# Optimization experiments

Hardware: AMD Instinct MI355X
Metric: run time of the kernel (lower is better)

The kernel has to match this reference:

```python
import jax, jax.numpy as jnp
import numpy as np

D_MODEL = 1024
N_HEADS = 16
HEAD_DIM = D_MODEL // N_HEADS  # 64
LATENT = 256
B, S = 2, 2048


def setup_inputs() -> dict:
    key = jax.random.key(0)
    ks = jax.random.split(key, 13)
    sc = 0.02
    inp = {
        'x': jax.random.normal(ks[0], (B, S, D_MODEL), jnp.float32),
        'Wq': jax.random.normal(ks[1], (D_MODEL, D_MODEL), jnp.float32) * sc,
        'bq': jnp.zeros((D_MODEL,), jnp.float32),
        'Wkd': jax.random.normal(ks[2], (D_MODEL, LATENT), jnp.float32) * sc,
        'bkd': jnp.zeros((LATENT,), jnp.float32),
        'Wvd': jax.random.normal(ks[3], (D_MODEL, LATENT), jnp.float32) * sc,
        'bvd': jnp.zeros((LATENT,), jnp.float32),
        'Wku': jax.random.normal(ks[4], (LATENT, D_MODEL), jnp.float32) * sc,
        'bku': jnp.zeros((D_MODEL,), jnp.float32),
        'Wvu': jax.random.normal(ks[5], (LATENT, D_MODEL), jnp.float32) * sc,
        'bvu': jnp.zeros((D_MODEL,), jnp.float32),
        'Wo': jax.random.normal(ks[6], (D_MODEL, D_MODEL), jnp.float32) * sc,
        'bo': jnp.zeros((D_MODEL,), jnp.float32),
    }
    return inp


def reference(x, Wq, bq, Wkd, bkd, Wvd, bvd, Wku, bku, Wvu, bvu, Wo, bo):
    b, s, _ = x.shape
    # projections
    Q = x @ Wq + bq                      # [b, s, d_model]
    K_latent = x @ Wkd + bkd             # [b, s, latent]
    V_latent = x @ Wvd + bvd             # [b, s, latent]
    K = K_latent @ Wku + bku             # [b, s, d_model]
    V = V_latent @ Wvu + bvu             # [b, s, d_model]
    # split heads
    Qh = Q.reshape(b, s, N_HEADS, HEAD_DIM)
    Kh = K.reshape(b, s, N_HEADS, HEAD_DIM)
    Vh = V.reshape(b, s, N_HEADS, HEAD_DIM)
    scale = 1.0 / jnp.sqrt(jnp.asarray(HEAD_DIM, x.dtype))
    scores = jnp.einsum('bqhd,bkhd->bhqk', Qh, Kh) * scale  # [b,h,s,s]
    attn = jax.nn.softmax(scores, axis=-1)
    ctx = jnp.einsum('bhqk,bkhd->bqhd', attn, Vh).reshape(b, s, D_MODEL)
    out = ctx @ Wo + bo
    return out
```

## Files before the change

kernel.cpp:

```cpp
#include <hip/hip_runtime.h>
#include <hip/hip_bf16.h>
#include <cstddef>

#define B_SZ 2
#define SEQ  2048
#define DM   1024
#define NH   16
#define HD   64
#define LAT  256
#define MTOT (B_SZ*SEQ)
#define NQKV 1536
#define QSCALE 0.18033688011112042f

typedef short bf16x8 __attribute__((ext_vector_type(8)));
typedef float floatx4 __attribute__((ext_vector_type(4)));
typedef float floatx16 __attribute__((ext_vector_type(16)));
typedef unsigned short u16;

#if __has_builtin(__builtin_amdgcn_exp2f)
#define EXP2(x) __builtin_amdgcn_exp2f(x)
#else
#define EXP2(x) exp2f(x)
#endif

__device__ __forceinline__ u16 f2bf(float f) {
  union { float f; unsigned u; } a; a.f = f;
  unsigned r = a.u + 0x7FFFu + ((a.u >> 16) & 1u);
  return (u16)(r >> 16);
}

__device__ __forceinline__ floatx4 mfma16(bf16x8 a, bf16x8 b, floatx4 c) {
  return __builtin_amdgcn_mfma_f32_16x16x32_bf16(a, b, c, 0, 0, 0);
}

__device__ __forceinline__ floatx16 mfma32(bf16x8 a, bf16x8 b, floatx16 c) {
  return __builtin_amdgcn_mfma_f32_32x32x16_bf16(a, b, c, 0, 0, 0);
}

__device__ __forceinline__ void load16(const u16* g, u16* l) {
  __builtin_amdgcn_global_load_lds((const __attribute__((address_space(1))) unsigned*)g,
                                   (__attribute__((address_space(3))) unsigned*)l, 16, 0, 0);
}

__device__ void transpose_tile(const float* __restrict__ W, u16* __restrict__ WT,
                               int K, int N, int k0, int n0, u16 (*t)[65]) {
  const int r = threadIdx.x >> 4;
  const int c4 = (threadIdx.x & 15) * 4;
#pragma unroll
  for (int s = 0; s < 4; s++) {
    int row = s * 16 + r;
    float4 v = *(const float4*)&W[(size_t)(k0 + row) * N + n0 + c4];
    t[row][c4 + 0] = f2bf(v.x); t[row][c4 + 1] = f2bf(v.y);
    t[row][c4 + 2] = f2bf(v.z); t[row][c4 + 3] = f2bf(v.w);
  }
  __syncthreads();
  const int r2 = threadIdx.x >> 2;
  const int c8 = (threadIdx.x & 3) * 16;
  __align__(16) u16 tmp[16];
#pragma unroll
  for (int i = 0; i < 16; i++) tmp[i] = t[c8 + i][r2];
  u16* dst = WT + (size_t)(n0 + r2) * K + k0 + c8;
  *(bf16x8*)dst       = *(const bf16x8*)&tmp[0];
  *(bf16x8*)(dst + 8) = *(const bf16x8*)&tmp[8];
}

__global__ __launch_bounds__(256)
void prep_k(const float* __restrict__ x, u16* __restrict__ xb,
            const float* __restrict__ Wq, const float* __restrict__ Wkd,
            const float* __restrict__ Wvd, const float* __restrict__ Wku,
            const float* __restrict__ Wvu, const float* __restrict__ Wo,
            u16* __restrict__ WstkT, u16* __restrict__ WkuT,
            u16* __restrict__ WvuT, u16* __restrict__ WoT,
            const float* __restrict__ bq, const float* __restrict__ bkd,
            const float* __restrict__ bvd, float* __restrict__ bqkv) {
  __shared__ u16 t[64][65];
  const int blk = blockIdx.x;
  if (blk < 4096) {
    int i = blk * 256 + threadIdx.x;
    float4 v = ((const float4*)x)[i];
    ushort4 o; o.x = f2bf(v.x); o.y = f2bf(v.y); o.z = f2bf(v.z); o.w = f2bf(v.w);
    ((ushort4*)xb)[i] = o;
  } else if (blk < 4352) {
    int tt = blk - 4096;
    transpose_tile(Wq, WstkT, DM, DM, (tt >> 4) * 64, (tt & 15) * 64, t);
  } else if (blk < 4416) {
    int tt = blk - 4352;
    transpose_tile(Wkd, WstkT + (size_t)DM * DM, DM, LAT, (tt >> 2) * 64, (tt & 3) * 64, t);
  } else if (blk < 4480) {
    int tt = blk - 4416;
    transpose_tile(Wvd, WstkT + (size_t)1280 * DM, DM, LAT, (tt >> 2) * 64, (tt & 3) * 64, t);
  } else if (blk < 4544) {
    int tt = blk - 4480;
    transpose_tile(Wku, WkuT, LAT, DM, (tt >> 4) * 64, (tt & 15) * 64, t);
  } else if (blk < 4608) {
    int tt = blk - 4544;
    transpose_tile(Wvu, WvuT, LAT, DM, (tt >> 4) * 64, (tt & 15) * 64, t);
  } else if (blk < 4864) {
    int tt = blk - 4608;
    transpose_tile(Wo, WoT, DM, DM, (tt >> 4) * 64, (tt & 15) * 64, t);
  } else {
    int i = (blk - 4864) * 256 + threadIdx.x;
    float v = (i < 1024) ? bq[i] : (i < 1280) ? bkd[i - 1024] : bvd[i - 1280];
    bqkv[i] = v;
  }
}

template<int TM, int OUT_BF16, int VT1>
__global__ __launch_bounds__(256)
void gemm_bt(const u16* __restrict__ A0, const u16* __restrict__ A1,
             const u16* __restrict__ BT0, const u16* __restrict__ BT1,
             const float* __restrict__ bias0, const float* __restrict__ bias1,
             void* __restrict__ C0, void* __restrict__ C1,
             int M, int N, int Kd, int lda, float qscale, int qcols) {
  constexpr int FM = TM / 32;
  __shared__ u16 As[TM * 64];
  __shared__ u16 Bs[64 * 64];
  const u16* A  = blockIdx.z ? A1 : A0;
  const u16* BT = blockIdx.z ? BT1 : BT0;
  const float* bias = blockIdx.z ? bias1 : bias0;
  void* C = blockIdx.z ? C1 : C0;

  const int tid = threadIdx.x;
  const int m0 = blockIdx.y * TM, n0 = blockIdx.x * 64;
  const int wave = tid >> 6, lane = tid & 63;
  const int l15 = lane & 15, quad = lane >> 4;
  const int wm = (wave >> 1) * (TM / 2), wn = (wave & 1) * 32;

  floatx4 acc[FM][2];
#pragma unroll
  for (int i = 0; i < FM; i++)
#pragma unroll
    for (int j = 0; j < 2; j++) acc[i][j] = (floatx4){0.f, 0.f, 0.f, 0.f};

  const int tr = tid >> 3;
  const int tc8 = (tid & 7) * 8;
  const u16* Ag = A  + (size_t)(m0 + tr) * lda + tc8;
  const u16* Bg = BT + (size_t)(n0 + tr) * Kd + tc8;
  u16* AsW = &As[(size_t)tid * 8];
  u16* BsW = &Bs[(size_t)tid * 8];

  for (int k0 = 0; k0 < Kd; k0 += 64) {
    __syncthreads();
#pragma unroll
    for (int s = 0; s < FM; s++)
      load16(Ag + (size_t)(s * 32) * lda + k0, AsW + s * 2048);
#pragma unroll
    for (int s = 0; s < 2; s++)
      load16(Bg + (size_t)(s * 32) * Kd  + k0, BsW + s * 2048);
    __syncthreads();
#pragma unroll
    for (int kk = 0; kk < 2; kk++) {
      bf16x8 af[FM], bfr[2];
#pragma unroll
      for (int i = 0; i < FM; i++)
        af[i]  = *(const bf16x8*)&As[(wm + i * 16 + l15) * 64 + kk * 32 + quad * 8];
#pragma unroll
      for (int j = 0; j < 2; j++)
        bfr[j] = *(const bf16x8*)&Bs[(wn + j * 16 + l15) * 64 + kk * 32 + quad * 8];
#pragma unroll
      for (int i = 0; i < FM; i++)
#pragma unroll
        for (int j = 0; j < 2; j++)
          acc[i][j] = mfma16(af[i], bfr[j], acc[i][j]);
    }
  }

  if (VT1 && blockIdx.z == 1) {
#pragma unroll
    for (int i = 0; i < FM; i++) {
      int row = m0 + wm + i * 16 + quad * 4;
      int bb = row >> 11, sb = row & 2047;
#pragma unroll
      for (int j = 0; j < 2; j++) {
        int col = n0 + wn + j * 16 + l15;
        float bv = bias[col];
        union { u16 u[4]; uint2 w2; } tv;
#pragma unroll
        for (int r = 0; r < 4; r++) tv.u[r] = f2bf(acc[i][j][r] + bv);
        *(uint2*)((u16*)C + ((size_t)(bb * 16 + (col >> 6)) * 64 + (col & 63)) * SEQ + sb) = tv.w2;
      }
    }
  } else {
#pragma unroll
    for (int i = 0; i < FM; i++) {
      int row = m0 + wm + i * 16 + quad * 4;
#pragma unroll
      for (int j = 0; j < 2; j++) {
        int col = n0 + wn + j * 16 + l15;
        float bv = bias[col];
        float sc = (col < qcols) ? qscale : 1.f;
#pragma unroll
        for (int r = 0; r < 4; r++) {
          float v = (acc[i][j][r] + bv) * sc;
          if (OUT_BF16) ((u16*)C)[(size_t)(row + r) * N + col] = f2bf(v);
          else          ((float*)C)[(size_t)(row + r) * N + col] = v;
        }
      }
    }
  }
}

__global__ __launch_bounds__(512, 3)
void attn_fused(const u16* __restrict__ Q, const u16* __restrict__ K,
                const u16* __restrict__ VT, u16* __restrict__ CTX) {
  __shared__ __align__(16) u16 KVt[2][2][2][64][64];
  const int lin = blockIdx.y * gridDim.x + blockIdx.x;
  const int idx = lin >> 3;
  const int bh = (lin & 7) * 4 + (idx >> 4);
  const int q0 = (idx & 15) * 128;
  const int b = bh >> 4, h = bh & 15;
  const int wave = threadIdx.x >> 6, lane = threadIdx.x & 63;
  const int qw = wave & 3;
  const int kw = wave >> 2;
  const int l31 = lane & 31;
  const int hi = lane >> 5;
  const int lr = lane >> 3;
  const int cx = (lane & 7) ^ lr;

  bf16x8 qf[4];
  {
    const u16* Qp = Q + (size_t)(b * SEQ + q0 + qw * 32 + l31) * NQKV + h * HD + hi * 8;
#pragma unroll
    for (int dc = 0; dc < 4; dc++)
      qf[dc] = *(const bf16x8*)(Qp + dc * 16);
  }

  const u16* Ks[2];
  const u16* Vs[2];
#pragma unroll
  for (int s = 0; s < 2; s++) {
    int r = qw * 8 + s * 32 + lr;
    Ks[s] = K + (size_t)(b * SEQ + kw * 1024 + r) * DM + h * HD + cx * 8;
    Vs[s] = VT + ((size_t)bh * HD + r) * SEQ + kw * 1024 + cx * 8;
  }

  floatx16 o[2];
  const floatx16 zf16 = {0.f,0.f,0.f,0.f,0.f,0.f,0.f,0.f,0.f,0.f,0.f,0.f,0.f,0.f,0.f,0.f};
  o[0] = zf16; o[1] = zf16;
  float ls = 0.f;

#pragma unroll
  for (int s = 0; s < 2; s++) {
    load16(Ks[s], &KVt[kw][0][0][qw * 8 + s * 32][0]);
    load16(Vs[s], &KVt[kw][0][1][qw * 8 + s * 32][0]);
  }
  __syncthreads();

#pragma unroll 2
  for (int t = 0; t < 16; ++t) {
    const int cur = t & 1, nxt = cur ^ 1;
    if (t < 15) {
      const int kt = (t + 1) * 64;
#pragma unroll
      for (int s = 0; s < 2; s++) {
        load16(Ks[s] + (size_t)kt * DM, &KVt[kw][nxt][0][qw * 8 + s * 32][0]);
        load16(Vs[s] + kt,              &KVt[kw][nxt][1][qw * 8 + s * 32][0]);
      }
    }
#pragma unroll
    for (int kh = 0; kh < 2; kh++) {
      const int rk = kh * 32 + l31;
      bf16x8 kf[4];
#pragma unroll
      for (int dc = 0; dc < 4; dc++)
        kf[dc] = *(const bf16x8*)&KVt[kw][cur][0][rk][((dc * 2 + hi) ^ (rk & 7)) * 8];
      floatx16 z = zf16;
      __builtin_amdgcn_s_setprio(1);
#pragma unroll
      for (int dc = 0; dc < 4; dc++) z = mfma32(kf[dc], qf[dc], z);
      __builtin_amdgcn_s_setprio(0);
      {
        float p0 = EXP2(z[0]), p1 = EXP2(z[1]), p2 = EXP2(z[2]), p3 = EXP2(z[3]);
        float p4 = EXP2(z[4]), p5 = EXP2(z[5]), p6 = EXP2(z[6]), p7 = EXP2(z[7]);
        ls += ((p0 + p1) + (p2 + p3)) + ((p4 + p5) + (p6 + p7));
        unsigned w0 = __builtin_amdgcn_perm(__float_as_uint(p1) + 0x8000u,
                                            __float_as_uint(p0) + 0x8000u, 0x07060302u);
        unsigned w1 = __builtin_amdgcn_perm(__float_as_uint(p3) + 0x8000u,
                                            __float_as_uint(p2) + 0x8000u, 0x07060302u);
        unsigned w2 = __builtin_amdgcn_perm(__float_as_uint(p5) + 0x8000u,
                                            __float_as_uint(p4) + 0x8000u, 0x07060302u);
        unsigned w3 = __builtin_amdgcn_perm(__float_as_uint(p7) + 0x8000u,
                                            __float_as_uint(p6) + 0x8000u, 0x07060302u);
        unsigned s0 = (unsigned)__shfl_xor((int)w0, 32);
        unsigned s1 = (unsigned)__shfl_xor((int)w1, 32);
        unsigned s2 = (unsigned)__shfl_xor((int)w2, 32);
        unsigned s3 = (unsigned)__shfl_xor((int)w3, 32);
        union { unsigned u[4]; bf16x8 v; } b0;
        b0.u[0] = hi ? s2 : w0;
        b0.u[1] = hi ? s3 : w1;
        b0.u[2] = hi ? w2 : s0;
        b0.u[3] = hi ? w3 : s1;
        bf16x8 vf0 = *(const bf16x8*)&KVt[kw][cur][1][l31     ][((kh * 4 + hi) ^ (l31 & 7)) * 8];
        bf16x8 vf1 = *(const bf16x8*)&KVt[kw][cur][1][32 + l31][((kh * 4 + hi) ^ (l31 & 7)) * 8];
        __builtin_amdgcn_s_setprio(1);
        o[0] = mfma32(vf0, b0.v, o[0]);
        o[1] = mfma32(vf1, b0.v, o[1]);
        __builtin_amdgcn_s_setprio(0);
      }
      {
        float p0 = EXP2(z[8]),  p1 = EXP2(z[9]),  p2 = EXP2(z[10]), p3 = EXP2(z[11]);
        float p4 = EXP2(z[12]), p5 = EXP2(z[13]), p6 = EXP2(z[14]), p7 = EXP2(z[15]);
        ls += ((p0 + p1) + (p2 + p3)) + ((p4 + p5) + (p6 + p7));
        unsigned w0 = __builtin_amdgcn_perm(__float_as_uint(p1) + 0x8000u,
                                            __float_as_uint(p0) + 0x8000u, 0x07060302u);
        unsigned w1 = __builtin_amdgcn_perm(__float_as_uint(p3) + 0x8000u,
                                            __float_as_uint(p2) + 0x8000u, 0x07060302u);
        unsigned w2 = __builtin_amdgcn_perm(__float_as_uint(p5) + 0x8000u,
                                            __float_as_uint(p4) + 0x8000u, 0x07060302u);
        unsigned w3 = __builtin_amdgcn_perm(__float_as_uint(p7) + 0x8000u,
                                            __float_as_uint(p6) + 0x8000u, 0x07060302u);
        unsigned s0 = (unsigned)__shfl_xor((int)w0, 32);
        unsigned s1 = (unsigned)__shfl_xor((int)w1, 32);
        unsigned s2 = (unsigned)__shfl_xor((int)w2, 32);
        unsigned s3 = (unsigned)__shfl_xor((int)w3, 32);
        union { unsigned u[4]; bf16x8 v; } b1;
        b1.u[0] = hi ? s2 : w0;
        b1.u[1] = hi ? s3 : w1;
        b1.u[2] = hi ? w2 : s0;
        b1.u[3] = hi ? w3 : s1;
        bf16x8 vf0 = *(const bf16x8*)&KVt[kw][cur][1][l31     ][((kh * 4 + 2 + hi) ^ (l31 & 7)) * 8];
        bf16x8 vf1 = *(const bf16x8*)&KVt[kw][cur][1][32 + l31][((kh * 4 + 2 + hi) ^ (l31 & 7)) * 8];
        __builtin_amdgcn_s_setprio(1);
        o[0] = mfma32(vf0, b1.v, o[0]);
        o[1] = mfma32(vf1, b1.v, o[1]);
        __builtin_amdgcn_s_setprio(0);
      }
    }
    __syncthreads();
  }

  float* Osh = (float*)&KVt[0][0][0][0][0];
  float* Lsh = Osh + 128 * 68;
  const float lsum = ls + __shfl_xor(ls, 32);
  const int q = qw * 32 + l31;
  if (kw == 1) {
#pragma unroll
    for (int dh = 0; dh < 2; dh++)
#pragma unroll
      for (int g = 0; g < 4; g++) {
        floatx4 tv = {o[dh][4 * g], o[dh][4 * g + 1], o[dh][4 * g + 2], o[dh][4 * g + 3]};
        *(floatx4*)&Osh[q * 68 + dh * 32 + g * 8 + hi * 4] = tv;
      }
    if (hi == 0) Lsh[q] = lsum;
  }
  __syncthreads();
  if (kw == 0) {
    const float inv = 1.f / (lsum + Lsh[q]);
    u16* Crow = CTX + (size_t)(b * SEQ + q0 + q) * DM + h * HD + hi * 4;
#pragma unroll
    for (int dh = 0; dh < 2; dh++)
#pragma unroll
      for (int g = 0; g < 4; g++) {
        const float* oc = &Osh[q * 68 + dh * 32 + g * 8 + hi * 4];
        union { u16 u[4]; uint2 w2; } tv;
#pragma unroll
        for (int r = 0; r < 4; r++)
          tv.u[r] = f2bf((o[dh][4 * g + r] + oc[r]) * inv);
        *(uint2*)(Crow + dh * 32 + g * 8) = tv.w2;
      }
  }
}

extern "C" void kernel_launch(void* const* d_in, const int* in_sizes, int n_in,
                              void* d_out, int out_size, void* d_ws, size_t ws_size,
                              hipStream_t stream) {
  const float* x   = (const float*)d_in[0];
  const float* Wq  = (const float*)d_in[1];
  const float* bq  = (const float*)d_in[2];
  const float* Wkd = (const float*)d_in[3];
  const float* bkd = (const float*)d_in[4];
  const float* Wvd = (const float*)d_in[5];
  const float* bvd = (const float*)d_in[6];
  const float* Wku = (const float*)d_in[7];
  const float* bku = (const float*)d_in[8];
  const float* Wvu = (const float*)d_in[9];
  const float* bvu = (const float*)d_in[10];
  const float* Wo  = (const float*)d_in[11];
  const float* bo  = (const float*)d_in[12];
  float* out = (float*)d_out;

  float* bqkv = (float*)d_ws;
  u16* p = (u16*)((char*)d_ws + 1536 * sizeof(float));
  u16* xb    = p; p += (size_t)MTOT * DM;
  u16* WstkT = p; p += (size_t)NQKV * DM;
  u16* WkuT  = p; p += (size_t)DM * LAT;
  u16* WvuT  = p; p += (size_t)DM * LAT;
  u16* WoT   = p; p += (size_t)DM * DM;
  u16* QKVb  = p; p += (size_t)MTOT * NQKV;
  u16* Kb    = p; p += (size_t)MTOT * DM;
  u16* VTb   = p; p += (size_t)MTOT * DM;
  u16* CXb   = p; p += (size_t)MTOT * DM;

  prep_k<<<4870, 256, 0, stream>>>(x, xb, Wq, Wkd, Wvd, Wku, Wvu, Wo,
                                   WstkT, WkuT, WvuT, WoT, bq, bkd, bvd, bqkv);

  gemm_bt<128, 1, 0><<<dim3(NQKV / 64, MTOT / 128, 1), 256, 0, stream>>>(
      xb, xb, WstkT, WstkT, bqkv, bqkv, QKVb, QKVb, MTOT, NQKV, DM, DM, QSCALE, DM);
  gemm_bt<128, 1, 1><<<dim3(DM / 64, MTOT / 128, 2), 256, 0, stream>>>(
      QKVb + 1024, QKVb + 1280, WkuT, WvuT, bku, bvu, Kb, VTb, MTOT, DM, LAT, NQKV, 1.f, 0);

  attn_fused<<<dim3(SEQ / 128, B_SZ * NH), 512, 0, stream>>>(QKVb, Kb, VTb, CXb);

  gemm_bt<64, 0, 0><<<dim3(DM / 64, MTOT / 64, 1), 256, 0, stream>>>(
      CXb, CXb, WoT, WoT, bo, bo, out, out, MTOT, DM, DM, DM, 1.f, 0);
}
```

Measured before the change: 207.0 us.

## Give each attention wave two query sub-tiles to reuse K/V fragments

Halves the attention block from 512 to 256 threads, so each wave now handles 64 query rows (two 32-row sub-tiles) instead of 32. Each K and V fragment read from LDS feeds twice as many MFMAs, and each thread issues four async loads per tile instead of two. The aim is less LDS read traffic per FLOP and fewer waves contending per block. The cost is higher register pressure (four output accumulators, two score tiles), fewer waves to hide latency, and a changed launch bound of (256, 2).

New measurement: 204.7 us. Within noise of the previous version (-1.1%).

```diff
diff --git a/kernel.cpp b/kernel.cpp
--- a/kernel.cpp
+++ b/kernel.cpp
@@ -40,6 +40,28 @@
 __device__ __forceinline__ void load16(const u16* g, u16* l) {
   __builtin_amdgcn_global_load_lds((const __attribute__((address_space(1))) unsigned*)g,
                                    (__attribute__((address_space(3))) unsigned*)l, 16, 0, 0);
+}
+
+__device__ __forceinline__ bf16x8 packex(float p0, float p1, float p2, float p3,
+                                         float p4, float p5, float p6, float p7, int hi) {
+  unsigned w0 = __builtin_amdgcn_perm(__float_as_uint(p1) + 0x8000u,
+                                      __float_as_uint(p0) + 0x8000u, 0x07060302u);
+  unsigned w1 = __builtin_amdgcn_perm(__float_as_uint(p3) + 0x8000u,
+                                      __float_as_uint(p2) + 0x8000u, 0x07060302u);
+  unsigned w2 = __builtin_amdgcn_perm(__float_as_uint(p5) + 0x8000u,
+                                      __float_as_uint(p4) + 0x8000u, 0x07060302u);
+  unsigned w3 = __builtin_amdgcn_perm(__float_as_uint(p7) + 0x8000u,
+                                      __float_as_uint(p6) + 0x8000u, 0x07060302u);
+  unsigned s0 = (unsigned)__shfl_xor((int)w0, 32);
+  unsigned s1 = (unsigned)__shfl_xor((int)w1, 32);
+  unsigned s2 = (unsigned)__shfl_xor((int)w2, 32);
+  unsigned s3 = (unsigned)__shfl_xor((int)w3, 32);
+  union { unsigned u[4]; bf16x8 v; } bb;
+  bb.u[0] = hi ? s2 : w0;
+  bb.u[1] = hi ? s3 : w1;
+  bb.u[2] = hi ? w2 : s0;
+  bb.u[3] = hi ? w3 : s1;
+  return bb.v;
 }
 
 __device__ void transpose_tile(const float* __restrict__ W, u16* __restrict__ WT,
@@ -200,7 +222,7 @@
   }
 }
 
-__global__ __launch_bounds__(512, 3)
+__global__ __launch_bounds__(256, 2)
 void attn_fused(const u16* __restrict__ Q, const u16* __restrict__ K,
                 const u16* __restrict__ VT, u16* __restrict__ CTX) {
   __shared__ __align__(16) u16 KVt[2][2][2][64][64];
@@ -210,39 +232,35 @@
   const int q0 = (idx & 15) * 128;
   const int b = bh >> 4, h = bh & 15;
   const int wave = threadIdx.x >> 6, lane = threadIdx.x & 63;
-  const int qw = wave & 3;
-  const int kw = wave >> 2;
+  const int qw = wave & 1;
+  const int kw = wave >> 1;
   const int l31 = lane & 31;
   const int hi = lane >> 5;
   const int lr = lane >> 3;
   const int cx = (lane & 7) ^ lr;
 
-  bf16x8 qf[4];
+  bf16x8 qf0[4], qf1[4];
   {
-    const u16* Qp = Q + (size_t)(b * SEQ + q0 + qw * 32 + l31) * NQKV + h * HD + hi * 8;
-#pragma unroll
-    for (int dc = 0; dc < 4; dc++)
-      qf[dc] = *(const bf16x8*)(Qp + dc * 16);
-  }
-
-  const u16* Ks[2];
-  const u16* Vs[2];
-#pragma unroll
-  for (int s = 0; s < 2; s++) {
-    int r = qw * 8 + s * 32 + lr;
-    Ks[s] = K + (size_t)(b * SEQ + kw * 1024 + r) * DM + h * HD + cx * 8;
-    Vs[s] = VT + ((size_t)bh * HD + r) * SEQ + kw * 1024 + cx * 8;
-  }
-
-  floatx16 o[2];
+    const u16* Qp = Q + (size_t)(b * SEQ + q0 + qw * 64 + l31) * NQKV + h * HD + hi * 8;
+#pragma unroll
+    for (int dc = 0; dc < 4; dc++) {
+      qf0[dc] = *(const bf16x8*)(Qp + dc * 16);
+      qf1[dc] = *(const bf16x8*)(Qp + (size_t)32 * NQKV + dc * 16);
+    }
+  }
+
+  const u16* Kbase = K + (size_t)(b * SEQ + kw * 1024 + qw * 32 + lr) * DM + h * HD + cx * 8;
+  const u16* Vbase = VT + ((size_t)bh * HD + qw * 32 + lr) * SEQ + kw * 1024 + cx * 8;
+
+  floatx16 o00, o01, o10, o11;
   const floatx16 zf16 = {0.f,0.f,0.f,0.f,0.f,0.f,0.f,0.f,0.f,0.f,0.f,0.f,0.f,0.f,0.f,0.f};
-  o[0] = zf16; o[1] = zf16;
-  float ls = 0.f;
-
-#pragma unroll
-  for (int s = 0; s < 2; s++) {
-    load16(Ks[s], &KVt[kw][0][0][qw * 8 + s * 32][0]);
-    load16(Vs[s], &KVt[kw][0][1][qw * 8 + s * 32][0]);
+  o00 = zf16; o01 = zf16; o10 = zf16; o11 = zf16;
+  float ls0 = 0.f, ls1 = 0.f;
+
+#pragma unroll
+  for (int s = 0; s < 4; s++) {
+    load16(Kbase + (size_t)(s * 8) * DM, &KVt[kw][0][0][qw * 32 + s * 8][0]);
+    load16(Vbase + (size_t)(s * 8) * SEQ, &KVt[kw][0][1][qw * 32 + s * 8][0]);
   }
   __syncthreads();
 
@@ -252,9 +270,9 @@
     if (t < 15) {
       const int kt = (t + 1) * 64;
 #pragma unroll
-      for (int s = 0; s < 2; s++) {
-        load16(Ks[s] + (size_t)kt * DM, &KVt[kw][nxt][0][qw * 8 + s * 32][0]);
-        load16(Vs[s] + kt,              &KVt[kw][nxt][1][qw * 8 + s * 32][0]);
+      for (int s = 0; s < 4; s++) {
+        load16(Kbase + (size_t)(kt + s * 8) * DM, &KVt[kw][nxt][0][qw * 32 + s * 8][0]);
+        load16(Vbase + (size_t)(s * 8) * SEQ + kt, &KVt[kw][nxt][1][qw * 32 + s * 8][0]);
       }
     }
 #pragma unroll
@@ -264,65 +282,48 @@
 #pragma unroll
       for (int dc = 0; dc < 4; dc++)
         kf[dc] = *(const bf16x8*)&KVt[kw][cur][0][rk][((dc * 2 + hi) ^ (rk & 7)) * 8];
-      floatx16 z = zf16;
+      floatx16 z0 = zf16, z1 = zf16;
       __builtin_amdgcn_s_setprio(1);
 #pragma unroll
-      for (int dc = 0; dc < 4; dc++) z = mfma32(kf[dc], qf[dc], z);
+      for (int dc = 0; dc < 4; dc++) {
+        z0 = mfma32(kf[dc], qf0[dc], z0);
+        z1 = mfma32(kf[dc], qf1[dc], z1);
+      }
       __builtin_amdgcn_s_setprio(0);
+      bf16x8 vfA0 = *(const bf16x8*)&KVt[kw][cur][1][l31     ][((kh * 4 + hi) ^ (l31 & 7)) * 8];
+      bf16x8 vfA1 = *(const bf16x8*)&KVt[kw][cur][1][32 + l31][((kh * 4 + hi) ^ (l31 & 7)) * 8];
+      bf16x8 vfB0 = *(const bf16x8*)&KVt[kw][cur][1][l31     ][((kh * 4 + 2 + hi) ^ (l31 & 7)) * 8];
+      bf16x8 vfB1 = *(const bf16x8*)&KVt[kw][cur][1][32 + l31][((kh * 4 + 2 + hi) ^ (l31 & 7)) * 8];
       {
-        float p0 = EXP2(z[0]), p1 = EXP2(z[1]), p2 = EXP2(z[2]), p3 = EXP2(z[3]);
-        float p4 = EXP2(z[4]), p5 = EXP2(z[5]), p6 = EXP2(z[6]), p7 = EXP2(z[7]);
-        ls += ((p0 + p1) + (p2 + p3)) + ((p4 + p5) + (p6 + p7));
-        unsigned w0 = __builtin_amdgcn_perm(__float_as_uint(p1) + 0x8000u,
-                                            __float_as_uint(p0) + 0x8000u, 0x07060302u);
-        unsigned w1 = __builtin_amdgcn_perm(__float_as_uint(p3) + 0x8000u,
-                                            __float_as_uint(p2) + 0x8000u, 0x07060302u);
-        unsigned w2 = __builtin_amdgcn_perm(__float_as_uint(p5) + 0x8000u,
-                                            __float_as_uint(p4) + 0x8000u, 0x07060302u);
-        unsigned w3 = __builtin_amdgcn_perm(__float_as_uint(p7) + 0x8000u,
-                                            __float_as_uint(p6) + 0x8000u, 0x07060302u);
-        unsigned s0 = (unsigned)__shfl_xor((int)w0, 32);
-        unsigned s1 = (unsigned)__shfl_xor((int)w1, 32);
-        unsigned s2 = (unsigned)__shfl_xor((int)w2, 32);
-        unsigned s3 = (unsigned)__shfl_xor((int)w3, 32);
-        union { unsigned u[4]; bf16x8 v; } b0;
-        b0.u[0] = hi ? s2 : w0;
-        b0.u[1] = hi ? s3 : w1;
-        b0.u[2] = hi ? w2 : s0;
-        b0.u[3] = hi ? w3 : s1;
-        bf16x8 vf0 = *(const bf16x8*)&KVt[kw][cur][1][l31     ][((kh * 4 + hi) ^ (l31 & 7)) * 8];
-        bf16x8 vf1 = *(const bf16x8*)&KVt[kw][cur][1][32 + l31][((kh * 4 + hi) ^ (l31 & 7)) * 8];
+        float p0 = EXP2(z0[0]), p1 = EXP2(z0[1]), p2 = EXP2(z0[2]), p3 = EXP2(z0[3]);
+        float p4 = EXP2(z0[4]), p5 = EXP2(z0[5]), p6 = EXP2(z0[6]), p7 = EXP2(z0[7]);
+        float p8 = EXP2(z0[8]),  p9 = EXP2(z0[9]),  pa = EXP2(z0[10]), pb = EXP2(z0[11]);
+        float pc = EXP2(z0[12]), pd = EXP2(z0[13]), pe = EXP2(z0[14]), pf = EXP2(z0[15]);
+        ls0 += (((p0 + p1) + (p2 + p3)) + ((p4 + p5) + (p6 + p7)))
+             + (((p8 + p9) + (pa + pb)) + ((pc + pd) + (pe + pf)));
+        bf16x8 bA = packex(p0, p1, p2, p3, p4, p5, p6, p7, hi);
+        bf16x8 bB = packex(p8, p9, pa, pb, pc, pd, pe, pf, hi);
         __builtin_amdgcn_s_setprio(1);
-        o[0] = mfma32(vf0, b0.v, o[0]);
-        o[1] = mfma32(vf1, b0.v, o[1]);
+        o00 = mfma32(vfA0, bA, o00);
+        o01 = mfma32(vfA1, bA, o01);
+        o00 = mfma32(vfB0, bB, o00);
+        o01 = mfma32(vfB1, bB, o01);
         __builtin_amdgcn_s_setprio(0);
       }
       {
-        float p0 = EXP2(z[8]),  p1 = EXP2(z[9]),  p2 = EXP2(z[10]), p3 = EXP2(z[11]);
-        float p4 = EXP2(z[12]), p5 = EXP2(z[13]), p6 = EXP2(z[14]), p7 = EXP2(z[15]);
-        ls += ((p0 + p1) + (p2 + p3)) + ((p4 + p5) + (p6 + p7));
-        unsigned w0 = __builtin_amdgcn_perm(__float_as_uint(p1) + 0x8000u,
-                                            __float_as_uint(p0) + 0x8000u, 0x07060302u);
-        unsigned w1 = __builtin_amdgcn_perm(__float_as_uint(p3) + 0x8000u,
-                                            __float_as_uint(p2) + 0x8000u, 0x07060302u);
-        unsigned w2 = __builtin_amdgcn_perm(__float_as_uint(p5) + 0x8000u,
-                                            __float_as_uint(p4) + 0x8000u, 0x07060302u);
-        unsigned w3 = __builtin_amdgcn_perm(__float_as_uint(p7) + 0x8000u,
-                                            __float_as_uint(p6) + 0x8000u, 0x07060302u);
-        unsigned s0 = (unsigned)__shfl_xor((int)w0, 32);
-        unsigned s1 = (unsigned)__shfl_xor((int)w1, 32);
-        unsigned s2 = (unsigned)__shfl_xor((int)w2, 32);
-        unsigned s3 = (unsigned)__shfl_xor((int)w3, 32);
-        union { unsigned u[4]; bf16x8 v; } b1;
-        b1.u[0] = hi ? s2 : w0;
-        b1.u[1] = hi ? s3 : w1;
-        b1.u[2] = hi ? w2 : s0;
-        b1.u[3] = hi ? w3 : s1;
-        bf16x8 vf0 = *(const bf16x8*)&KVt[kw][cur][1][l31     ][((kh * 4 + 2 + hi) ^ (l31 & 7)) * 8];
-        bf16x8 vf1 = *(const bf16x8*)&KVt[kw][cur][1][32 + l31][((kh * 4 + 2 + hi) ^ (l31 & 7)) * 8];
+        float p0 = EXP2(z1[0]), p1 = EXP2(z1[1]), p2 = EXP2(z1[2]), p3 = EXP2(z1[3]);
+        float p4 = EXP2(z1[4]), p5 = EXP2(z1[5]), p6 = EXP2(z1[6]), p7 = EXP2(z1[7]);
+        float p8 = EXP2(z1[8]),  p9 = EXP2(z1[9]),  pa = EXP2(z1[10]), pb = EXP2(z1[11]);
+        float pc = EXP2(z1[12]), pd = EXP2(z1[13]), pe = EXP2(z1[14]), pf = EXP2(z1[15]);
+        ls1 += (((p0 + p1) + (p2 + p3)) + ((p4 + p5) + (p6 + p7)))
+             + (((p8 + p9) + (pa + pb)) + ((pc + pd) + (pe + pf)));
+        bf16x8 bA = packex(p0, p1, p2, p3, p4, p5, p6, p7, hi);
+        bf16x8 bB = packex(p8, p9, pa, pb, pc, pd, pe, pf, hi);
         __builtin_amdgcn_s_setprio(1);
-        o[0] = mfma32(vf0, b1.v, o[0]);
-        o[1] = mfma32(vf1, b1.v, o[1]);
+        o10 = mfma32(vfA0, bA, o10);
+        o11 = mfma32(vfA1, bA, o11);
+        o10 = mfma32(vfB0, bB, o10);
+        o11 = mfma32(vfB1, bB, o11);
         __builtin_amdgcn_s_setprio(0);
       }
     }
@@ -331,33 +332,49 @@
 
   float* Osh = (float*)&KVt[0][0][0][0][0];
   float* Lsh = Osh + 128 * 68;
-  const float lsum = ls + __shfl_xor(ls, 32);
-  const int q = qw * 32 + l31;
+  const float lsum0 = ls0 + __shfl_xor(ls0, 32);
+  const float lsum1 = ls1 + __shfl_xor(ls1, 32);
+  const int qA = qw * 64 + l31;
+  const int qB = qw * 64 + 32 + l31;
   if (kw == 1) {
 #pragma unroll
-    for (int dh = 0; dh < 2; dh++)
-#pragma unroll
-      for (int g = 0; g < 4; g++) {
-        floatx4 tv = {o[dh][4 * g], o[dh][4 * g + 1], o[dh][4 * g + 2], o[dh][4 * g + 3]};
-        *(floatx4*)&Osh[q * 68 + dh * 32 + g * 8 + hi * 4] = tv;
-      }
-    if (hi == 0) Lsh[q] = lsum;
+    for (int g = 0; g < 4; g++) {
+      *(floatx4*)&Osh[qA * 68 +      g * 8 + hi * 4] =
+          (floatx4){o00[4*g], o00[4*g+1], o00[4*g+2], o00[4*g+3]};
+      *(floatx4*)&Osh[qA * 68 + 32 + g * 8 + hi * 4] =
+          (floatx4){o01[4*g], o01[4*g+1], o01[4*g+2], o01[4*g+3]};
+      *(floatx4*)&Osh[qB * 68 +      g * 8 + hi * 4] =
+          (floatx4){o10[4*g], o10[4*g+1], o10[4*g+2], o10[4*g+3]};
+      *(floatx4*)&Osh[qB * 68 + 32 + g * 8 + hi * 4] =
+          (floatx4){o11[4*g], o11[4*g+1], o11[4*g+2], o11[4*g+3]};
+    }
+    if (hi == 0) { Lsh[qA] = lsum0; Lsh[qB] = lsum1; }
   }
   __syncthreads();
   if (kw == 0) {
-    const float inv = 1.f / (lsum + Lsh[q]);
-    u16* Crow = CTX + (size_t)(b * SEQ + q0 + q) * DM + h * HD + hi * 4;
-#pragma unroll
-    for (int dh = 0; dh < 2; dh++)
-#pragma unroll
-      for (int g = 0; g < 4; g++) {
-        const float* oc = &Osh[q * 68 + dh * 32 + g * 8 + hi * 4];
-        union { u16 u[4]; uint2 w2; } tv;
-#pragma unroll
-        for (int r = 0; r < 4; r++)
-          tv.u[r] = f2bf((o[dh][4 * g + r] + oc[r]) * inv);
-        *(uint2*)(Crow + dh * 32 + g * 8) = tv.w2;
-      }
+    const float inv0 = 1.f / (lsum0 + Lsh[qA]);
+    const float inv1 = 1.f / (lsum1 + Lsh[qB]);
+    u16* CrowA = CTX + (size_t)(b * SEQ + q0 + qA) * DM + h * HD + hi * 4;
+    u16* CrowB = CTX + (size_t)(b * SEQ + q0 + qB) * DM + h * HD + hi * 4;
+#pragma unroll
+    for (int g = 0; g < 4; g++) {
+      const float* ocA0 = &Osh[qA * 68 +      g * 8 + hi * 4];
+      const float* ocA1 = &Osh[qA * 68 + 32 + g * 8 + hi * 4];
+      const float* ocB0 = &Osh[qB * 68 +      g * 8 + hi * 4];
+      const float* ocB1 = &Osh[qB * 68 + 32 + g * 8 + hi * 4];
+      union { u16 u[4]; uint2 w2; } t0, t1, t2, t3;
+#pragma unroll
+      for (int r = 0; r < 4; r++) {
+        t0.u[r] = f2bf((o00[4*g+r] + ocA0[r]) * inv0);
+        t1.u[r] = f2bf((o01[4*g+r] + ocA1[r]) * inv0);
+        t2.u[r] = f2bf((o10[4*g+r] + ocB0[r]) * inv1);
+        t3.u[r] = f2bf((o11[4*g+r] + ocB1[r]) * inv1);
+      }
+      *(uint2*)(CrowA +      g * 8) = t0.w2;
+      *(uint2*)(CrowA + 32 + g * 8) = t1.w2;
+      *(uint2*)(CrowB +      g * 8) = t2.w2;
+      *(uint2*)(CrowB + 32 + g * 8) = t3.w2;
+    }
   }
 }
 
@@ -399,7 +416,7 @@
   gemm_bt<128, 1, 1><<<dim3(DM / 64, MTOT / 128, 2), 256, 0, stream>>>(
       QKVb + 1024, QKVb + 1280, WkuT, WvuT, bku, bvu, Kb, VTb, MTOT, DM, LAT, NQKV, 1.f, 0);
 
-  attn_fused<<<dim3(SEQ / 128, B_SZ * NH), 512, 0, stream>>>(QKVb, Kb, VTb, CXb);
+  attn_fused<<<dim3(SEQ / 128, B_SZ * NH), 256, 0, stream>>>(QKVb, Kb, VTb, CXb);
 
   gemm_bt<64, 0, 0><<<dim3(DM / 64, MTOT / 64, 1), 256, 0, stream>>>(
       CXb, CXb, WoT, WoT, bo, bo, out, out, MTOT, DM, DM, DM, 1.f, 0);
```
